# Kernel optimization log

Hardware: AMD Instinct MI355X
Metric: run time of the kernel (lower is better)

The kernel has to match this reference:

```python
import jax, jax.numpy as jnp
import numpy as np

B, T, X, E, H, L = 4096, 32, 256, 32, 512, 2  # batch, theta_size, x_size, n_masks, hidden, num_hidden_layers


def _prelu(v, a):
    # PReLU with per-channel slope a (broadcast [E,H] or [B,E,H] vs [B,E,H])
    return jnp.where(v >= 0, v, a * v)


def setup_inputs() -> dict:
    key = jax.random.key(0)
    ks = jax.random.split(key, 12)
    theta = jax.random.normal(ks[0], (B, T), dtype=jnp.float32)
    x = jax.random.normal(ks[1], (B, X), dtype=jnp.float32)
    masks = jax.random.randint(ks[2], (E, T), 0, 2, dtype=jnp.int32)
    masks = masks.at[:, 0].set(1)  # guarantee non-empty subsets
    D = T + X
    s_in = 1.0 / np.sqrt(D)
    s_h = 1.0 / np.sqrt(H)
    # first Linear, split into theta-part and x-part of the weight matrix
    W1t = jax.random.normal(ks[3], (E, T, H), dtype=jnp.float32) * s_in
    W1x = jax.random.normal(ks[4], (E, X, H), dtype=jnp.float32) * s_in
    b1 = jax.random.normal(ks[5], (E, H), dtype=jnp.float32) * s_in
    a1 = jnp.full((E, H), 0.25, dtype=jnp.float32)  # PReLU init
    # num_layers hidden Linear(H,H) + PReLU
    Wh = jax.random.normal(ks[6], (L, E, H, H), dtype=jnp.float32) * s_h
    bh = jax.random.normal(ks[7], (L, E, H), dtype=jnp.float32) * s_h
    ah = jnp.full((L, E, H), 0.25, dtype=jnp.float32)
    # output Linear(H, 1) -> squeeze(-1)
    Wo = jax.random.normal(ks[8], (E, H), dtype=jnp.float32) * s_h
    bo = jax.random.normal(ks[9], (E,), dtype=jnp.float32) * s_h
    return {"theta": theta, "x": x, "masks": masks, "W1t": W1t, "W1x": W1x,
            "b1": b1, "a1": a1, "Wh": Wh, "bh": bh, "ah": ah, "Wo": Wo, "bo": bo}


def reference(theta, x, masks, W1t, W1x, b1, a1, Wh, bh, ah, Wo, bo):
    # theta[..., mask] followed by Linear is equivalent to masking theta per
    # expert and contracting with the full per-expert theta weight block.
    m = masks.astype(theta.dtype)                      # [E, T]
    tm = theta[:, None, :] * m[None, :, :]             # [B, E, T]
    h = (jnp.einsum('bet,eth->beh', tm, W1t)
         + jnp.einsum('bx,exh->beh', x, W1x) + b1)     # [B, E, H]
    h = _prelu(h, a1)
    for i in range(Wh.shape[0]):                       # small fixed layer loop
        h = jnp.einsum('beh,ehk->bek', h, Wh[i]) + bh[i]
        h = _prelu(h, ah[i])
    # Linear(H,1).squeeze(-1), stacked over masks on the last dim -> [B, E]
    return jnp.einsum('beh,eh->be', h, Wo) + bo
```

## Files before the change

### kernel.cpp

```cpp
#include <hip/hip_runtime.h>
#include <stdint.h>

#define B_SZ 4096
#define T_SZ 32
#define X_SZ 256
#define E_SZ 32
#define H_SZ 512
#define BM   64
#define AROW 1040
#define D_SZ 288

typedef __attribute__((ext_vector_type(8))) short  short8;
typedef __attribute__((ext_vector_type(4))) float  floatx4;

__device__ __forceinline__ unsigned short f2bf(float f) {
  unsigned u = __float_as_uint(f);
  u += 0x7fffu + ((u >> 16) & 1u);
  return (unsigned short)(u >> 16);
}
__device__ __forceinline__ unsigned pk2(float a, float b) {
  return (unsigned)f2bf(a) | ((unsigned)f2bf(b) << 16);
}

#define LPITCH 524

__global__ __launch_bounds__(256) void prep4_kernel(
    const float* __restrict__ W1t, const float* __restrict__ W1x,
    const int* __restrict__ masks, const float* __restrict__ Wh,
    const float* __restrict__ theta, const float* __restrict__ x,
    uint4* __restrict__ wcat, uint4* __restrict__ whf,
    unsigned short* __restrict__ tx) {
  const int bid = blockIdx.x, t = threadIdx.x;
  if (bid >= 1312) {
    int g = bid - 1312;
    int r = g * 64 + (t >> 2), c = t & 3;
    {
      float4 a = *(const float4*)(theta + (size_t)r * T_SZ + c * 8);
      float4 b = *(const float4*)(theta + (size_t)r * T_SZ + c * 8 + 4);
      *(uint4*)(tx + (size_t)r * D_SZ + c * 8) =
          make_uint4(pk2(a.x, a.y), pk2(a.z, a.w), pk2(b.x, b.y), pk2(b.z, b.w));
    }
#pragma unroll
    for (int j = 0; j < 8; ++j) {
      float4 a = *(const float4*)(x + (size_t)r * X_SZ + c * 64 + j * 8);
      float4 b = *(const float4*)(x + (size_t)r * X_SZ + c * 64 + j * 8 + 4);
      *(uint4*)(tx + (size_t)r * D_SZ + T_SZ + c * 64 + j * 8) =
          make_uint4(pk2(a.x, a.y), pk2(a.z, a.w), pk2(b.x, b.y), pk2(b.z, b.w));
    }
    return;
  }
  __shared__ unsigned short lds[32 * LPITCH];
  const int xcd = bid & 7, j = bid >> 3;
  const int q41 = j / 41;
  const int c   = j - q41 * 41;
  const int e   = xcd * 4 + (3 - q41);
  float4 v[16];
  if (c < 9) {
#pragma unroll
    for (int p = 0; p < 16; ++p) {
      int f  = p * 256 + t;
      int kk = f >> 7, n = (f & 127) * 4;
      int k  = c * 32 + kk;
      if (k < T_SZ) {
        v[p] = *(const float4*)(W1t + ((size_t)e * T_SZ + k) * H_SZ + n);
        float m = (float)masks[e * T_SZ + k];
        v[p].x *= m; v[p].y *= m; v[p].z *= m; v[p].w *= m;
      } else {
        v[p] = *(const float4*)(W1x + ((size_t)e * X_SZ + (k - T_SZ)) * H_SZ + n);
      }
    }
  } else {
    int h = c - 9, le = h >> 4, kt = h & 15;
    const float* base = Wh + (size_t)(le * E_SZ + e) * H_SZ * H_SZ +
                        (size_t)kt * 32 * H_SZ;
#pragma unroll
    for (int p = 0; p < 16; ++p) {
      int f  = p * 256 + t;
      int kk = f >> 7, n = (f & 127) * 4;
      v[p] = *(const float4*)(base + (size_t)kk * H_SZ + n);
    }
  }
#pragma unroll
  for (int p = 0; p < 16; ++p) {
    int f  = p * 256 + t;
    int kk = f >> 7, n = (f & 127) * 4;
    *(uint2*)&lds[kk * LPITCH + n] =
        make_uint2(pk2(v[p].x, v[p].y), pk2(v[p].z, v[p].w));
  }
  __syncthreads();
  uint4* dst = (c < 9)
                   ? (wcat + ((size_t)e * 9 + c) * 2048)
                   : (whf + ((size_t)(((c - 9) >> 4) * E_SZ + e) * 16 +
                             ((c - 9) & 15)) * 2048);
#pragma unroll 2
  for (int p = 0; p < 8; ++p) {
    int u  = p * 256 + t;
    int nb = u >> 6, l = u & 63;
    int n  = nb * 16 + (l & 15);
    int k0 = (l >> 4) * 8;
    unsigned d[4];
#pragma unroll
    for (int jj = 0; jj < 4; ++jj) {
      unsigned lo = lds[(k0 + 2 * jj)     * LPITCH + n];
      unsigned hi = lds[(k0 + 2 * jj + 1) * LPITCH + n];
      d[jj] = lo | (hi << 16);
    }
    dst[u] = make_uint4(d[0], d[1], d[2], d[3]);
  }
}

template <int NKT>
__device__ __forceinline__ void gemm_run(const char* smA, const short8* wp,
                                         int l16, int quad,
                                         floatx4 (&acc)[4][4]) {
#pragma unroll
  for (int mb = 0; mb < 4; ++mb)
#pragma unroll
    for (int i = 0; i < 4; ++i) acc[mb][i] = (floatx4)(0.f);
  short8 buf[2][4];
#pragma unroll
  for (int i = 0; i < 4; ++i) buf[0][i] = wp[i * 64];
#pragma unroll
  for (int kt = 0; kt < NKT; ++kt) {
    int nk = (kt + 1 < NKT) ? kt + 1 : kt;
    short8* nb = buf[(kt + 1) & 1];
#pragma unroll
    for (int i = 0; i < 4; ++i) nb[i] = wp[(size_t)nk * 2048 + i * 64];
    short8 af[4];
#pragma unroll
    for (int mb = 0; mb < 4; ++mb)
      af[mb] = *(const short8*)(smA + (mb * 16 + l16) * AROW + kt * 64 + quad * 16);
    const short8* cb = buf[kt & 1];
#pragma unroll
    for (int mb = 0; mb < 4; ++mb)
#pragma unroll
      for (int i = 0; i < 4; ++i)
        acc[mb][i] = __builtin_amdgcn_mfma_f32_16x16x32_bf16(af[mb], cb[i],
                                                             acc[mb][i], 0, 0, 0);
  }
}

__global__ __launch_bounds__(512, 4) void mlp_kernel(
    const unsigned short* __restrict__ tx,
    const short8* __restrict__ wcat, const short8* __restrict__ whf,
    const float* __restrict__ b1, const float* __restrict__ a1,
    const float* __restrict__ bh, const float* __restrict__ ah,
    const float* __restrict__ Wo, const float* __restrict__ bo,
    float* __restrict__ out, int phase) {
  __shared__ __align__(16) char smA[BM * AROW];
  const int tid = threadIdx.x;
  const int bid = blockIdx.x;
  const int e   = (bid & 7) * 4 + phase;
  const int m0  = (bid >> 3) * BM;
  const int w   = tid >> 6, l = tid & 63, l16 = l & 15, quad = l >> 4;

  {
    int r = tid >> 3, c = tid & 7;
    const unsigned short* src = tx + (size_t)(m0 + r) * D_SZ;
#pragma unroll
    for (int p = 0; p < 9; ++p)
      *(uint2*)(smA + r * AROW + 8 * (c + 8 * p)) =
          *(const uint2*)(src + 4 * (c + 8 * p));
  }
  __syncthreads();

  floatx4 acc[4][4];

  auto epi_store = [&](const float* bias, const float* slope) {
    float bb[4], aa[4];
#pragma unroll
    for (int i = 0; i < 4; ++i) {
      int col = w * 64 + i * 16 + l16;
      bb[i] = bias[col];
      aa[i] = slope[col];
    }
    __syncthreads();
#pragma unroll
    for (int mb = 0; mb < 4; ++mb) {
#pragma unroll
      for (int i = 0; i < 4; ++i) {
        unsigned dw[4];
#pragma unroll
        for (int r = 0; r < 4; ++r) {
          float v = acc[mb][i][r] + bb[i];
          v = v >= 0.f ? v : aa[i] * v;
          float o  = __shfl_xor(v, 1, 64);
          float lo = (l16 & 1) ? o : v;
          float hi = (l16 & 1) ? v : o;
          dw[r] = pk2(lo, hi);
        }
        int col2  = w * 64 + i * 16 + (l16 & ~1);
        int rbase = (l16 & 1) * 2;
#pragma unroll
        for (int rr = 0; rr < 2; ++rr) {
          int row = mb * 16 + quad * 4 + rbase + rr;
          *(unsigned*)(smA + row * AROW + col2 * 2) = dw[rbase + rr];
        }
      }
    }
    __syncthreads();
  };

  const int woff = w * 256 + l;
  gemm_run<9>(smA, wcat + (size_t)e * 9 * 2048 + woff, l16, quad, acc);
  epi_store(b1 + (size_t)e * H_SZ, a1 + (size_t)e * H_SZ);
  gemm_run<16>(smA, whf + (size_t)e * 16 * 2048 + woff, l16, quad, acc);
  epi_store(bh + (size_t)e * H_SZ, ah + (size_t)e * H_SZ);
  gemm_run<16>(smA, whf + (size_t)(E_SZ + e) * 16 * 2048 + woff, l16, quad, acc);
  {
    float bb[4], aa[4], wo[4];
#pragma unroll
    for (int i = 0; i < 4; ++i) {
      int col = w * 64 + i * 16 + l16;
      bb[i] = bh[(size_t)(E_SZ + e) * H_SZ + col];
      aa[i] = ah[(size_t)(E_SZ + e) * H_SZ + col];
      wo[i] = Wo[(size_t)e * H_SZ + col];
    }
    float ps[4][4];
#pragma unroll
    for (int mb = 0; mb < 4; ++mb)
#pragma unroll
      for (int r = 0; r < 4; ++r) ps[mb][r] = 0.f;
#pragma unroll
    for (int mb = 0; mb < 4; ++mb)
#pragma unroll
      for (int i = 0; i < 4; ++i)
#pragma unroll
        for (int r = 0; r < 4; ++r) {
          float v = acc[mb][i][r] + bb[i];
          v = v >= 0.f ? v : aa[i] * v;
          ps[mb][r] += v * wo[i];
        }
#pragma unroll
    for (int d = 1; d < 16; d <<= 1)
#pragma unroll
      for (int mb = 0; mb < 4; ++mb)
#pragma unroll
        for (int r = 0; r < 4; ++r) ps[mb][r] += __shfl_xor(ps[mb][r], d, 64);
    __syncthreads();
    float* scratch = (float*)smA;
    if (l16 == 0) {
#pragma unroll
      for (int mb = 0; mb < 4; ++mb)
#pragma unroll
        for (int r = 0; r < 4; ++r)
          scratch[(mb * 16 + quad * 4 + r) * 8 + w] = ps[mb][r];
    }
    __syncthreads();
    if (tid < BM) {
      float s = 0.f;
#pragma unroll
      for (int ww = 0; ww < 8; ++ww) s += scratch[tid * 8 + ww];
      out[(size_t)(m0 + tid) * E_SZ + e] = s + bo[e];
    }
  }
}

extern "C" void kernel_launch(void* const* d_in, const int* in_sizes, int n_in,
                              void* d_out, int out_size, void* d_ws, size_t ws_size,
                              hipStream_t stream) {
  const float* theta = (const float*)d_in[0];
  const float* x     = (const float*)d_in[1];
  const int*   masks = (const int*)d_in[2];
  const float* W1t   = (const float*)d_in[3];
  const float* W1x   = (const float*)d_in[4];
  const float* b1    = (const float*)d_in[5];
  const float* a1    = (const float*)d_in[6];
  const float* Wh    = (const float*)d_in[7];
  const float* bh    = (const float*)d_in[8];
  const float* ah    = (const float*)d_in[9];
  const float* Wo    = (const float*)d_in[10];
  const float* bo    = (const float*)d_in[11];
  float* out = (float*)d_out;

  uint4* wcat = (uint4*)d_ws;
  uint4* whf  = (uint4*)((char*)d_ws + (size_t)E_SZ * 9 * 2048 * 16);
  unsigned short* tx =
      (unsigned short*)((char*)d_ws + (size_t)E_SZ * 9 * 2048 * 16 +
                        (size_t)2 * E_SZ * 16 * 2048 * 16);

  prep4_kernel<<<1376, 256, 0, stream>>>(W1t, W1x, masks, Wh, theta, x,
                                         wcat, whf, tx);
  for (int p = 0; p < 4; ++p)
    mlp_kernel<<<512, 512, 0, stream>>>(tx, (const short8*)wcat,
                                        (const short8*)whf, b1, a1, bh, ah, Wo,
                                        bo, out, p);
}
```

Measured before the change: 326.2 us.

## Fuse four expert-phase launches into one persistent loop and double-buffer A fragments

The four per-phase mlp_kernel launches are merged into a single launch in which each block loops over its four experts, reloading the input tile into LDS each iteration. This removes three kernel launches and their tail/ramp gaps. The GEMM inner loop now prefetches the next k-tile's LDS A fragments alongside the B fragments, which raises register pressure. The prep kernel's LDS pitch changes to 526 with 32-bit stores to avoid bank conflicts, and the added per-block serialization may reduce overlap between experts.

```diff
diff --git a/kernel.cpp b/kernel.cpp
--- a/kernel.cpp
+++ b/kernel.cpp
@@ -22,9 +22,9 @@
   return (unsigned)f2bf(a) | ((unsigned)f2bf(b) << 16);
 }
 
-#define LPITCH 524
-
-__global__ __launch_bounds__(256) void prep4_kernel(
+#define LPITCH 526
+
+__global__ __launch_bounds__(256) void prep5_kernel(
     const float* __restrict__ W1t, const float* __restrict__ W1x,
     const int* __restrict__ masks, const float* __restrict__ Wh,
     const float* __restrict__ theta, const float* __restrict__ x,
@@ -80,12 +80,14 @@
       v[p] = *(const float4*)(base + (size_t)kk * H_SZ + n);
     }
   }
+  unsigned* lds32 = (unsigned*)lds;
 #pragma unroll
   for (int p = 0; p < 16; ++p) {
     int f  = p * 256 + t;
     int kk = f >> 7, n = (f & 127) * 4;
-    *(uint2*)&lds[kk * LPITCH + n] =
-        make_uint2(pk2(v[p].x, v[p].y), pk2(v[p].z, v[p].w));
+    int di = (kk * LPITCH + n) >> 1;
+    lds32[di]     = pk2(v[p].x, v[p].y);
+    lds32[di + 1] = pk2(v[p].z, v[p].w);
   }
   __syncthreads();
   uint4* dst = (c < 9)
@@ -117,25 +119,28 @@
   for (int mb = 0; mb < 4; ++mb)
 #pragma unroll
     for (int i = 0; i < 4; ++i) acc[mb][i] = (floatx4)(0.f);
-  short8 buf[2][4];
-#pragma unroll
-  for (int i = 0; i < 4; ++i) buf[0][i] = wp[i * 64];
+  short8 b[2][4], a[2][4];
+#pragma unroll
+  for (int i = 0; i < 4; ++i) b[0][i] = wp[i * 64];
+#pragma unroll
+  for (int mb = 0; mb < 4; ++mb)
+    a[0][mb] = *(const short8*)(smA + (mb * 16 + l16) * AROW + quad * 16);
 #pragma unroll
   for (int kt = 0; kt < NKT; ++kt) {
-    int nk = (kt + 1 < NKT) ? kt + 1 : kt;
-    short8* nb = buf[(kt + 1) & 1];
-#pragma unroll
-    for (int i = 0; i < 4; ++i) nb[i] = wp[(size_t)nk * 2048 + i * 64];
-    short8 af[4];
+    const int cur = kt & 1, nxt = cur ^ 1;
+    const int kn  = (kt + 1 < NKT) ? kt + 1 : kt;
+#pragma unroll
+    for (int i = 0; i < 4; ++i) b[nxt][i] = wp[(size_t)kn * 2048 + i * 64];
 #pragma unroll
     for (int mb = 0; mb < 4; ++mb)
-      af[mb] = *(const short8*)(smA + (mb * 16 + l16) * AROW + kt * 64 + quad * 16);
-    const short8* cb = buf[kt & 1];
+      a[nxt][mb] =
+          *(const short8*)(smA + (mb * 16 + l16) * AROW + kn * 64 + quad * 16);
 #pragma unroll
     for (int mb = 0; mb < 4; ++mb)
 #pragma unroll
       for (int i = 0; i < 4; ++i)
-        acc[mb][i] = __builtin_amdgcn_mfma_f32_16x16x32_bf16(af[mb], cb[i],
+        acc[mb][i] = __builtin_amdgcn_mfma_f32_16x16x32_bf16(a[cur][mb],
+                                                             b[cur][i],
                                                              acc[mb][i], 0, 0, 0);
   }
 }
@@ -146,23 +151,12 @@
     const float* __restrict__ b1, const float* __restrict__ a1,
     const float* __restrict__ bh, const float* __restrict__ ah,
     const float* __restrict__ Wo, const float* __restrict__ bo,
-    float* __restrict__ out, int phase) {
+    float* __restrict__ out) {
   __shared__ __align__(16) char smA[BM * AROW];
   const int tid = threadIdx.x;
   const int bid = blockIdx.x;
-  const int e   = (bid & 7) * 4 + phase;
   const int m0  = (bid >> 3) * BM;
   const int w   = tid >> 6, l = tid & 63, l16 = l & 15, quad = l >> 4;
-
-  {
-    int r = tid >> 3, c = tid & 7;
-    const unsigned short* src = tx + (size_t)(m0 + r) * D_SZ;
-#pragma unroll
-    for (int p = 0; p < 9; ++p)
-      *(uint2*)(smA + r * AROW + 8 * (c + 8 * p)) =
-          *(const uint2*)(src + 4 * (c + 8 * p));
-  }
-  __syncthreads();
 
   floatx4 acc[4][4];
 
@@ -202,56 +196,72 @@
   };
 
   const int woff = w * 256 + l;
-  gemm_run<9>(smA, wcat + (size_t)e * 9 * 2048 + woff, l16, quad, acc);
-  epi_store(b1 + (size_t)e * H_SZ, a1 + (size_t)e * H_SZ);
-  gemm_run<16>(smA, whf + (size_t)e * 16 * 2048 + woff, l16, quad, acc);
-  epi_store(bh + (size_t)e * H_SZ, ah + (size_t)e * H_SZ);
-  gemm_run<16>(smA, whf + (size_t)(E_SZ + e) * 16 * 2048 + woff, l16, quad, acc);
-  {
-    float bb[4], aa[4], wo[4];
-#pragma unroll
-    for (int i = 0; i < 4; ++i) {
-      int col = w * 64 + i * 16 + l16;
-      bb[i] = bh[(size_t)(E_SZ + e) * H_SZ + col];
-      aa[i] = ah[(size_t)(E_SZ + e) * H_SZ + col];
-      wo[i] = Wo[(size_t)e * H_SZ + col];
-    }
-    float ps[4][4];
-#pragma unroll
-    for (int mb = 0; mb < 4; ++mb)
-#pragma unroll
-      for (int r = 0; r < 4; ++r) ps[mb][r] = 0.f;
-#pragma unroll
-    for (int mb = 0; mb < 4; ++mb)
-#pragma unroll
-      for (int i = 0; i < 4; ++i)
-#pragma unroll
-        for (int r = 0; r < 4; ++r) {
-          float v = acc[mb][i][r] + bb[i];
-          v = v >= 0.f ? v : aa[i] * v;
-          ps[mb][r] += v * wo[i];
-        }
-#pragma unroll
-    for (int d = 1; d < 16; d <<= 1)
+#pragma unroll 1
+  for (int p = 0; p < 4; ++p) {
+    const int e = (bid & 7) * 4 + p;
+    __syncthreads();
+    {
+      int r = tid >> 3, c = tid & 7;
+      const unsigned short* src = tx + (size_t)(m0 + r) * D_SZ;
+#pragma unroll
+      for (int q = 0; q < 9; ++q)
+        *(uint2*)(smA + r * AROW + 8 * (c + 8 * q)) =
+            *(const uint2*)(src + 4 * (c + 8 * q));
+    }
+    __syncthreads();
+
+    gemm_run<9>(smA, wcat + (size_t)e * 9 * 2048 + woff, l16, quad, acc);
+    epi_store(b1 + (size_t)e * H_SZ, a1 + (size_t)e * H_SZ);
+    gemm_run<16>(smA, whf + (size_t)e * 16 * 2048 + woff, l16, quad, acc);
+    epi_store(bh + (size_t)e * H_SZ, ah + (size_t)e * H_SZ);
+    gemm_run<16>(smA, whf + (size_t)(E_SZ + e) * 16 * 2048 + woff, l16, quad,
+                 acc);
+    {
+      float bb[4], aa[4], wo[4];
+#pragma unroll
+      for (int i = 0; i < 4; ++i) {
+        int col = w * 64 + i * 16 + l16;
+        bb[i] = bh[(size_t)(E_SZ + e) * H_SZ + col];
+        aa[i] = ah[(size_t)(E_SZ + e) * H_SZ + col];
+        wo[i] = Wo[(size_t)e * H_SZ + col];
+      }
+      float ps[4][4];
 #pragma unroll
       for (int mb = 0; mb < 4; ++mb)
 #pragma unroll
-        for (int r = 0; r < 4; ++r) ps[mb][r] += __shfl_xor(ps[mb][r], d, 64);
-    __syncthreads();
-    float* scratch = (float*)smA;
-    if (l16 == 0) {
+        for (int r = 0; r < 4; ++r) ps[mb][r] = 0.f;
 #pragma unroll
       for (int mb = 0; mb < 4; ++mb)
 #pragma unroll
-        for (int r = 0; r < 4; ++r)
-          scratch[(mb * 16 + quad * 4 + r) * 8 + w] = ps[mb][r];
-    }
-    __syncthreads();
-    if (tid < BM) {
-      float s = 0.f;
-#pragma unroll
-      for (int ww = 0; ww < 8; ++ww) s += scratch[tid * 8 + ww];
-      out[(size_t)(m0 + tid) * E_SZ + e] = s + bo[e];
+        for (int i = 0; i < 4; ++i)
+#pragma unroll
+          for (int r = 0; r < 4; ++r) {
+            float v = acc[mb][i][r] + bb[i];
+            v = v >= 0.f ? v : aa[i] * v;
+            ps[mb][r] += v * wo[i];
+          }
+#pragma unroll
+      for (int d = 1; d < 16; d <<= 1)
+#pragma unroll
+        for (int mb = 0; mb < 4; ++mb)
+#pragma unroll
+          for (int r = 0; r < 4; ++r) ps[mb][r] += __shfl_xor(ps[mb][r], d, 64);
+      __syncthreads();
+      float* scratch = (float*)smA;
+      if (l16 == 0) {
+#pragma unroll
+        for (int mb = 0; mb < 4; ++mb)
+#pragma unroll
+          for (int r = 0; r < 4; ++r)
+            scratch[(mb * 16 + quad * 4 + r) * 8 + w] = ps[mb][r];
+      }
+      __syncthreads();
+      if (tid < BM) {
+        float s = 0.f;
+#pragma unroll
+        for (int ww = 0; ww < 8; ++ww) s += scratch[tid * 8 + ww];
+        out[(size_t)(m0 + tid) * E_SZ + e] = s + bo[e];
+      }
     }
   }
 }
@@ -279,10 +289,9 @@
       (unsigned short*)((char*)d_ws + (size_t)E_SZ * 9 * 2048 * 16 +
                         (size_t)2 * E_SZ * 16 * 2048 * 16);
 
-  prep4_kernel<<<1376, 256, 0, stream>>>(W1t, W1x, masks, Wh, theta, x,
+  prep5_kernel<<<1376, 256, 0, stream>>>(W1t, W1x, masks, Wh, theta, x,
                                          wcat, whf, tx);
-  for (int p = 0; p < 4; ++p)
-    mlp_kernel<<<512, 512, 0, stream>>>(tx, (const short8*)wcat,
-                                        (const short8*)whf, b1, a1, bh, ah, Wo,
-                                        bo, out, p);
-}
+  mlp_kernel<<<512, 512, 0, stream>>>(tx, (const short8*)wcat,
+                                      (const short8*)whf, b1, a1, bh, ah, Wo,
+                                      bo, out);
+}
```

After: 364.6 us. 1.12x slower.
